# Kernel tuning notes

Hardware: AMD Instinct MI355X
Metric: run time of the kernel (lower is better)

The kernel has to match this reference:

```python
import jax, jax.numpy as jnp
import numpy as np

B, T, D, HEADS = 4, 2048, 2048, 16  # math requires T == D


def setup_inputs() -> dict:
    key = jax.random.key(0)
    k1, k2, k3 = jax.random.split(key, 3)
    scale = 1.0 / np.sqrt(D)
    x = jax.random.normal(k1, (B, T, D), dtype=jnp.float32)
    w_qk = jax.random.normal(k2, (2 * D, D), dtype=jnp.float32) * scale
    w_dense = jax.random.normal(k3, (D, D), dtype=jnp.float32) * scale
    b_dense = jnp.zeros((D,), dtype=jnp.float32)
    return {"x": x, "w_qk": w_qk, "w_dense": w_dense, "b_dense": b_dense}


def reference(x, w_qk, w_dense, b_dense):
    b, t, d = x.shape
    h = HEADS
    vh = d // h
    # to_q_k: Linear(d, 2d, bias=False); chunk into k0, v
    kv = jnp.einsum('btd,ed->bte', x, w_qk)          # [b,t,2d]
    k0, v = kv[..., :d], kv[..., d:]                 # each [b,t,d]
    scale_factor = 1.0 / jnp.sqrt(jnp.asarray(d * (d - 1) / 2, dtype=x.dtype))
    # k = k0.transpose(1,2) -> [b,d,t]; scores = k @ v^T -> [b,d,t] (t==d)
    s = jnp.einsum('bmi,bjm->bij', k0, v) * scale_factor   # [b,d,t]
    a = jax.nn.softmax(s, axis=-1)
    q = jnp.einsum('bit,btd->bid', a, v)             # [b,d,d]
    # q.transpose(0,1).chunk(h, dim=0) -> stack(dim=1) -> transpose(1,2) -> reshape
    qt = jnp.swapaxes(q, 0, 1)                       # [d, b, d]
    stk = qt.reshape(h, vh, b, d)                    # h chunks of [vh,b,d]
    stk = jnp.transpose(stk, (1, 0, 2, 3))           # stack(dim=1): [vh,h,b,d]
    stk = jnp.transpose(stk, (0, 2, 1, 3))           # transpose(1,2): [vh,b,h,d]
    out = stk.reshape(b, t, d)
    # dropout in eval mode == identity; to_dense Linear
    return jnp.einsum('btd,ed->bte', out, w_dense) + b_dense
```

## Files before the change

### kernel.cpp

```cpp
#include <hip/hip_runtime.h>
#include <stdint.h>
#include <math.h>


typedef __bf16 bf16x8 __attribute__((ext_vector_type(8)));
typedef float  f32x4  __attribute__((ext_vector_type(4)));

typedef __attribute__((address_space(3))) uint32_t lds_u32_t;
typedef __attribute__((address_space(1))) const uint32_t glb_u32_t;

__device__ __forceinline__ float bf2f(uint16_t u) {
  union { uint32_t i; float f; } c; c.i = ((uint32_t)u) << 16; return c.f;
}
__device__ __forceinline__ uint16_t f2bf(float f) {
  union { float f; uint32_t i; } c; c.f = f;
  uint32_t i = c.i;
  return (uint16_t)((i + 0x7fffu + ((i >> 16) & 1u)) >> 16);
}

__device__ __forceinline__ void glds16(const uint16_t* g, const char* l) {
  __builtin_amdgcn_global_load_lds((glb_u32_t*)g, (lds_u32_t*)l, 16, 0, 0);
}

#define SCHED0() __builtin_amdgcn_sched_barrier(0)
#define BARRIER() do { SCHED0(); __builtin_amdgcn_s_barrier(); SCHED0(); } while (0)
#define VMCNT(n_) asm volatile("s_waitcnt vmcnt(" #n_ ")")

#define NX4 4194304u
#define NW4 2097152u
#define ND4 1048576u
__global__ __launch_bounds__(256) void k_cast_all(
    const float* __restrict__ x, const float* __restrict__ wqk,
    const float* __restrict__ wd, uint16_t* __restrict__ dst) {
  uint32_t i = blockIdx.x * 256 + threadIdx.x;
  float4 v;
  if (i < NX4)            v = reinterpret_cast<const float4*>(x)[i];
  else if (i < NX4 + NW4) v = reinterpret_cast<const float4*>(wqk)[i - NX4];
  else                    v = reinterpret_cast<const float4*>(wd)[i - NX4 - NW4];
  ushort4 o;
  o.x = f2bf(v.x); o.y = f2bf(v.y); o.z = f2bf(v.z); o.w = f2bf(v.w);
  reinterpret_cast<ushort4*>(dst)[i] = o;
}

__device__ __forceinline__ void gemm256_core(
    const uint16_t* aR0, const uint16_t* aR1,
    const uint16_t* bR0, const uint16_t* bR1,
    int K, f32x4 acc[8][4])
{
  extern __shared__ uint4 smem_u4[];
  char* smem = (char*)smem_u4;
  const int tid = threadIdx.x;
  const int w = tid >> 6, l = tid & 63;
  const int wm = (w >> 2) * 128, wn = (w & 3) * 64;
  const int frow = l & 15, fkc = l >> 4;
  const uint32_t chunk = (uint32_t)((fkc ^ ((frow >> 1) & 3)) * 16);
  const uint32_t aBase = (uint32_t)(wm + frow) * 64 + chunk;
  const uint32_t bBase = 65536u + (uint32_t)(wn + frow) * 64 + chunk;
  char* lW = smem + (uint32_t)w * 1024u;
  const int NIT = K >> 7;

#define LDSA(kh_, buf_, half_) (lW + ((buf_) * 32768u + (kh_) * 16384u + (half_) * 8192u))
#define LDSB(kh_, buf_, half_) (lW + (65536u + (buf_) * 32768u + (kh_) * 16384u + (half_) * 8192u))
#define STG_A(off_, kh_, buf_) do { \
    glds16(aR0 + (off_), LDSA(kh_, buf_, 0)); \
    glds16(aR1 + (off_), LDSA(kh_, buf_, 1)); } while (0)
#define STG_B(off_, kh_, buf_) do { \
    glds16(bR0 + (off_), LDSB(kh_, buf_, 0)); \
    glds16(bR1 + (off_), LDSB(kh_, buf_, 1)); } while (0)
#define RD_A(mi_, kh_, buf_) \
    (*reinterpret_cast<const bf16x8*>(smem + (aBase + (mi_) * 1024u + (kh_) * 16384u + (buf_) * 32768u)))
#define RD_B(ni_, kh_, buf_) \
    (*reinterpret_cast<const bf16x8*>(smem + (bBase + (ni_) * 1024u + (kh_) * 16384u + (buf_) * 32768u)))
#define PH_RD12(kh_, buf_) do { \
    a0 = RD_A(0, kh_, buf_); a1 = RD_A(1, kh_, buf_); \
    a2 = RD_A(2, kh_, buf_); a3 = RD_A(3, kh_, buf_); \
    a4 = RD_A(4, kh_, buf_); a5 = RD_A(5, kh_, buf_); \
    a6 = RD_A(6, kh_, buf_); a7 = RD_A(7, kh_, buf_); \
    b0 = RD_B(0, kh_, buf_); b1 = RD_B(1, kh_, buf_); \
    b2 = RD_B(2, kh_, buf_); b3 = RD_B(3, kh_, buf_); } while (0)
#define MFMA8(ai_, mi_) do { \
    acc[mi_][0] = __builtin_amdgcn_mfma_f32_16x16x32_bf16(ai_, b0, acc[mi_][0], 0, 0, 0); \
    acc[mi_][1] = __builtin_amdgcn_mfma_f32_16x16x32_bf16(ai_, b1, acc[mi_][1], 0, 0, 0); \
    acc[mi_][2] = __builtin_amdgcn_mfma_f32_16x16x32_bf16(ai_, b2, acc[mi_][2], 0, 0, 0); \
    acc[mi_][3] = __builtin_amdgcn_mfma_f32_16x16x32_bf16(ai_, b3, acc[mi_][3], 0, 0, 0); \
  } while (0)
#define MFMA_PH() do { \
    BARRIER(); \
    __builtin_amdgcn_s_setprio(1); \
    MFMA8(a0, 0); MFMA8(a1, 1); MFMA8(a2, 2); MFMA8(a3, 3); \
    MFMA8(a4, 4); MFMA8(a5, 5); MFMA8(a6, 6); MFMA8(a7, 7); \
    __builtin_amdgcn_s_setprio(0); } while (0)

  STG_A(0, 0, 0); STG_B(0, 0, 0); STG_A(32, 1, 0); STG_B(32, 1, 0);
  STG_A(64, 0, 1); STG_B(64, 0, 1);
  VMCNT(8);

  bf16x8 a0, a1, a2, a3, a4, a5, a6, a7, b0, b1, b2, b3;
  BARRIER();

  for (int it = 0; it < NIT - 1; ++it) {
    PH_RD12(0, 0); STG_A(96, 1, 1);  STG_B(96, 1, 1);  VMCNT(8); MFMA_PH();
    PH_RD12(1, 0); STG_A(128, 0, 0); STG_B(128, 0, 0); VMCNT(8); MFMA_PH();
    PH_RD12(0, 1); STG_A(160, 1, 0); STG_B(160, 1, 0); VMCNT(8); MFMA_PH();
    PH_RD12(1, 1); STG_A(192, 0, 1); STG_B(192, 0, 1); VMCNT(8); MFMA_PH();
    aR0 += 128; aR1 += 128; bR0 += 128; bR1 += 128;
  }

  PH_RD12(0, 0); STG_A(96, 1, 1); STG_B(96, 1, 1); VMCNT(8); MFMA_PH();
  PH_RD12(1, 0); VMCNT(4); MFMA_PH();
  PH_RD12(0, 1); VMCNT(4); MFMA_PH();
  PH_RD12(1, 1); VMCNT(0); MFMA_PH();
#undef LDSA
#undef LDSB
#undef STG_A
#undef STG_B
#undef RD_A
#undef RD_B
#undef PH_RD12
#undef MFMA8
#undef MFMA_PH
}

__device__ __forceinline__ int stage_co() {
  const int tid = threadIdx.x;
  return (((tid & 3) ^ ((tid >> 3) & 3)) * 8);
}

__global__ __launch_bounds__(512, 2) void k_gemm_kv(
    const uint16_t* __restrict__ W,
    const uint16_t* __restrict__ X,
    uint16_t* __restrict__ k0T,
    uint16_t* __restrict__ vT)
{
  const int tid = threadIdx.x;
  const int bm = blockIdx.y, bn = blockIdx.x;
  const int r0 = tid >> 2, co = stage_co();
  const uint16_t* aR0 = W + (size_t)(bm * 256 + r0) * 2048 + co;
  const uint16_t* aR1 = W + (size_t)(bm * 256 + 128 + r0) * 2048 + co;
  const uint16_t* bR0 = X + (size_t)(bn * 256 + r0) * 2048 + co;
  const uint16_t* bR1 = X + (size_t)(bn * 256 + 128 + r0) * 2048 + co;
  f32x4 acc[8][4];
#pragma unroll
  for (int i = 0; i < 8; ++i)
#pragma unroll
    for (int j = 0; j < 4; ++j) acc[i][j] = (f32x4){0.f, 0.f, 0.f, 0.f};
  gemm256_core(aR0, aR1, bR0, bR1, 2048, acc);
  const int w = tid >> 6, l = tid & 63;
  const int wm = (w >> 2) * 128, wn = (w & 3) * 64;
  const int cr = (l >> 4) * 4, cc = l & 15;
  uint16_t* Cb = (bm < 8) ? k0T : vT;
  const int rb = (bm & 7) * 256;
#pragma unroll
  for (int mi = 0; mi < 8; ++mi)
#pragma unroll
    for (int ni = 0; ni < 4; ++ni)
#pragma unroll
      for (int g = 0; g < 4; ++g) {
        int lr = rb + wm + mi * 16 + cr + g;
        int bt = bn * 256 + wn + ni * 16 + cc;
        Cb[(size_t)lr * 8192 + bt] = f2bf(acc[mi][ni][g]);
      }
}

__global__ __launch_bounds__(512, 2) void k_gemm_bt(
    const uint16_t* __restrict__ A, int lda, long sA,
    const uint16_t* __restrict__ B, int ldb, long sB,
    uint16_t* __restrict__ C, int ldc, long sC,
    int K, float scale)
{
  const int z = blockIdx.z;
  A += (size_t)z * sA; B += (size_t)z * sB; C += (size_t)z * sC;
  const int tid = threadIdx.x;
  const int bm = blockIdx.y, bn = blockIdx.x;
  const int r0 = tid >> 2, co = stage_co();
  const uint16_t* aR0 = A + (size_t)(bm * 256 + r0) * lda + co;
  const uint16_t* aR1 = A + (size_t)(bm * 256 + 128 + r0) * lda + co;
  const uint16_t* bR0 = B + (size_t)(bn * 256 + r0) * ldb + co;
  const uint16_t* bR1 = B + (size_t)(bn * 256 + 128 + r0) * ldb + co;
  f32x4 acc[8][4];
#pragma unroll
  for (int i = 0; i < 8; ++i)
#pragma unroll
    for (int j = 0; j < 4; ++j) acc[i][j] = (f32x4){0.f, 0.f, 0.f, 0.f};
  gemm256_core(aR0, aR1, bR0, bR1, K, acc);
  const int w = tid >> 6, l = tid & 63;
  const int wm = (w >> 2) * 128, wn = (w & 3) * 64;
  const int cr = (l >> 4) * 4, cc = l & 15;
#pragma unroll
  for (int mi = 0; mi < 8; ++mi)
#pragma unroll
    for (int ni = 0; ni < 4; ++ni)
#pragma unroll
      for (int g = 0; g < 4; ++g) {
        int grow = bm * 256 + wm + mi * 16 + cr + g;
        int gcol = bn * 256 + wn + ni * 16 + cc;
        C[(size_t)grow * ldc + gcol] = f2bf(acc[mi][ni][g] * scale);
      }
}

__device__ __forceinline__ size_t qrow_off(int rr) {
  int bp = rr >> 11, tp = rr & 2047;
  int bi = (tp >> 4) & 3;
  int i  = (tp & 15) * 128 + bp * 32 + (tp >> 6);
  return ((size_t)bi * 2048 + (size_t)i) * 2048;
}

__global__ __launch_bounds__(512, 2) void k_gemm_out(
    const uint16_t* __restrict__ Q,
    const uint16_t* __restrict__ W,
    const float*    __restrict__ bias,
    float*          __restrict__ Out)
{
  const int tid = threadIdx.x;
  const int bm = blockIdx.y, bn = blockIdx.x;
  const int r0 = tid >> 2, co = stage_co();
  const uint16_t* aR0 = Q + qrow_off(bm * 256 + r0) + co;
  const uint16_t* aR1 = Q + qrow_off(bm * 256 + 128 + r0) + co;
  const uint16_t* bR0 = W + (size_t)(bn * 256 + r0) * 2048 + co;
  const uint16_t* bR1 = W + (size_t)(bn * 256 + 128 + r0) * 2048 + co;
  f32x4 acc[8][4];
#pragma unroll
  for (int i = 0; i < 8; ++i)
#pragma unroll
    for (int j = 0; j < 4; ++j) acc[i][j] = (f32x4){0.f, 0.f, 0.f, 0.f};
  gemm256_core(aR0, aR1, bR0, bR1, 2048, acc);
  const int w = tid >> 6, l = tid & 63;
  const int wm = (w >> 2) * 128, wn = (w & 3) * 64;
  const int cr = (l >> 4) * 4, cc = l & 15;
#pragma unroll
  for (int mi = 0; mi < 8; ++mi)
#pragma unroll
    for (int ni = 0; ni < 4; ++ni)
#pragma unroll
      for (int g = 0; g < 4; ++g) {
        int grow = bm * 256 + wm + mi * 16 + cr + g;
        int gcol = bn * 256 + wn + ni * 16 + cc;
        Out[(size_t)grow * 2048 + gcol] = acc[mi][ni][g] + bias[gcol];
      }
}

__global__ __launch_bounds__(256) void k_transpose(
    const uint16_t* __restrict__ src, uint16_t* __restrict__ dst)
{
  __shared__ uint16_t tile[64][65];
  const int tid = threadIdx.x;
  const int bx = blockIdx.x;
  const int by = blockIdx.y;
  const int cu = tid & 31, r0 = tid >> 5;
#pragma unroll
  for (int p = 0; p < 8; ++p) {
    int r = p * 8 + r0;
    uint32_t v = *reinterpret_cast<const uint32_t*>(
        &src[(size_t)(by * 64 + r) * 8192 + bx * 64 + cu * 2]);
    tile[r][cu * 2]     = (uint16_t)(v & 0xffffu);
    tile[r][cu * 2 + 1] = (uint16_t)(v >> 16);
  }
  __syncthreads();
#pragma unroll
  for (int p = 0; p < 8; ++p) {
    int r = p * 8 + r0;
    uint32_t lo = tile[cu * 2][r], hi = tile[cu * 2 + 1][r];
    *reinterpret_cast<uint32_t*>(
        &dst[(size_t)(bx * 64 + r) * 2048 + by * 64 + cu * 2]) = lo | (hi << 16);
  }
}

__global__ __launch_bounds__(256) void k_softmax(uint16_t* __restrict__ s)
{
  uint16_t* p = s + (size_t)blockIdx.x * 2048;
  const int tid = threadIdx.x;
  uint4 raw = reinterpret_cast<const uint4*>(p)[tid];
  uint32_t u[4] = {raw.x, raw.y, raw.z, raw.w};
  float x[8];
#pragma unroll
  for (int i = 0; i < 4; ++i) {
    x[2 * i]     = bf2f((uint16_t)(u[i] & 0xffffu));
    x[2 * i + 1] = bf2f((uint16_t)(u[i] >> 16));
  }
  float m = x[0];
#pragma unroll
  for (int i = 1; i < 8; ++i) m = fmaxf(m, x[i]);
#pragma unroll
  for (int o = 32; o; o >>= 1) m = fmaxf(m, __shfl_xor(m, o, 64));
  __shared__ float redm[4], reds[4];
  if ((tid & 63) == 0) redm[tid >> 6] = m;
  __syncthreads();
  m = fmaxf(fmaxf(redm[0], redm[1]), fmaxf(redm[2], redm[3]));
  float sum = 0.f;
#pragma unroll
  for (int i = 0; i < 8; ++i) { x[i] = __expf(x[i] - m); sum += x[i]; }
#pragma unroll
  for (int o = 32; o; o >>= 1) sum += __shfl_xor(sum, o, 64);
  if ((tid & 63) == 0) reds[tid >> 6] = sum;
  __syncthreads();
  sum = reds[0] + reds[1] + reds[2] + reds[3];
  float inv = 1.0f / sum;
  uint32_t ou[4];
#pragma unroll
  for (int i = 0; i < 4; ++i) {
    uint32_t lo = f2bf(x[2 * i] * inv);
    uint32_t hi = f2bf(x[2 * i + 1] * inv);
    ou[i] = lo | (hi << 16);
  }
  reinterpret_cast<uint4*>(p)[tid] = make_uint4(ou[0], ou[1], ou[2], ou[3]);
}

extern "C" void kernel_launch(void* const* d_in, const int* in_sizes, int n_in,
                              void* d_out, int out_size, void* d_ws, size_t ws_size,
                              hipStream_t stream) {
  const float* x       = (const float*)d_in[0];
  const float* w_qk    = (const float*)d_in[1];
  const float* w_dense = (const float*)d_in[2];
  const float* b_dense = (const float*)d_in[3];
  float* out = (float*)d_out;

  static int attr_done = 0;
  if (!attr_done) {
    (void)hipFuncSetAttribute(reinterpret_cast<const void*>(k_gemm_kv),
                              hipFuncAttributeMaxDynamicSharedMemorySize, 131072);
    (void)hipFuncSetAttribute(reinterpret_cast<const void*>(k_gemm_bt),
                              hipFuncAttributeMaxDynamicSharedMemorySize, 131072);
    (void)hipFuncSetAttribute(reinterpret_cast<const void*>(k_gemm_out),
                              hipFuncAttributeMaxDynamicSharedMemorySize, 131072);
    attr_done = 1;
  }

  const size_t NX = 4ull * 2048 * 2048;
  const size_t NW = 4096ull * 2048;
  const size_t ND = 2048ull * 2048;

  uint16_t* xb   = (uint16_t*)d_ws;
  uint16_t* wqkb = xb + NX;
  uint16_t* wdb  = wqkb + NW;
  uint16_t* k0T  = wdb + ND;
  uint16_t* vT   = k0T + NX;
  uint16_t* qb   = xb;
  uint16_t* Vn   = (uint16_t*)d_out;
  uint16_t* sb   = Vn + NX;

  const float scale = (float)(1.0 / sqrt(0.5 * 2048.0 * 2047.0));

  k_cast_all<<<dim3((NX4 + NW4 + ND4) / 256), 256, 0, stream>>>(x, w_qk, w_dense, xb);

  k_gemm_kv<<<dim3(32, 16), 512, 131072, stream>>>(wqkb, xb, k0T, vT);
  k_transpose<<<dim3(128, 32), 256, 0, stream>>>(vT, Vn);
  k_gemm_bt<<<dim3(8, 8, 4), 512, 131072, stream>>>(
      k0T, 8192, 2048L, Vn, 2048, 2048L * 2048L, sb, 2048, 2048L * 2048L, 2048, scale);
  k_softmax<<<dim3(8192), 256, 0, stream>>>(sb);
  k_gemm_bt<<<dim3(8, 8, 4), 512, 131072, stream>>>(
      sb, 2048, 2048L * 2048L, vT, 8192, 2048L, qb, 2048, 2048L * 2048L, 2048, 1.0f);
  k_gemm_out<<<dim3(8, 32), 512, 131072, stream>>>(qb, wdb, b_dense, out);
}
```

Baseline: 473.1 us.

## Software-pipeline LDS fragment reads with MFMAs across quarter-K stages in GEMM core

Restructures the 256x256 GEMM main loop so that LDS reads for the next K-slice are interleaved with the MFMAs of the current slice. B fragments are double-buffered in registers and each A fragment is reloaded right after its MFMA group. The staging pattern moves from two buffers of two halves to four quarter buffers, with one barrier per segment. The aim is to hide LDS read latency behind matrix math, at the cost of more live registers, which could pressure occupancy at 2 blocks per CU.

```diff
diff --git a/kernel.cpp b/kernel.cpp
--- a/kernel.cpp
+++ b/kernel.cpp
@@ -57,68 +57,83 @@
   const uint32_t aBase = (uint32_t)(wm + frow) * 64 + chunk;
   const uint32_t bBase = 65536u + (uint32_t)(wn + frow) * 64 + chunk;
   char* lW = smem + (uint32_t)w * 1024u;
-  const int NIT = K >> 7;
-
-#define LDSA(kh_, buf_, half_) (lW + ((buf_) * 32768u + (kh_) * 16384u + (half_) * 8192u))
-#define LDSB(kh_, buf_, half_) (lW + (65536u + (buf_) * 32768u + (kh_) * 16384u + (half_) * 8192u))
-#define STG_A(off_, kh_, buf_) do { \
-    glds16(aR0 + (off_), LDSA(kh_, buf_, 0)); \
-    glds16(aR1 + (off_), LDSA(kh_, buf_, 1)); } while (0)
-#define STG_B(off_, kh_, buf_) do { \
-    glds16(bR0 + (off_), LDSB(kh_, buf_, 0)); \
-    glds16(bR1 + (off_), LDSB(kh_, buf_, 1)); } while (0)
-#define RD_A(mi_, kh_, buf_) \
-    (*reinterpret_cast<const bf16x8*>(smem + (aBase + (mi_) * 1024u + (kh_) * 16384u + (buf_) * 32768u)))
-#define RD_B(ni_, kh_, buf_) \
-    (*reinterpret_cast<const bf16x8*>(smem + (bBase + (ni_) * 1024u + (kh_) * 16384u + (buf_) * 32768u)))
-#define PH_RD12(kh_, buf_) do { \
-    a0 = RD_A(0, kh_, buf_); a1 = RD_A(1, kh_, buf_); \
-    a2 = RD_A(2, kh_, buf_); a3 = RD_A(3, kh_, buf_); \
-    a4 = RD_A(4, kh_, buf_); a5 = RD_A(5, kh_, buf_); \
-    a6 = RD_A(6, kh_, buf_); a7 = RD_A(7, kh_, buf_); \
-    b0 = RD_B(0, kh_, buf_); b1 = RD_B(1, kh_, buf_); \
-    b2 = RD_B(2, kh_, buf_); b3 = RD_B(3, kh_, buf_); } while (0)
-#define MFMA8(ai_, mi_) do { \
-    acc[mi_][0] = __builtin_amdgcn_mfma_f32_16x16x32_bf16(ai_, b0, acc[mi_][0], 0, 0, 0); \
-    acc[mi_][1] = __builtin_amdgcn_mfma_f32_16x16x32_bf16(ai_, b1, acc[mi_][1], 0, 0, 0); \
-    acc[mi_][2] = __builtin_amdgcn_mfma_f32_16x16x32_bf16(ai_, b2, acc[mi_][2], 0, 0, 0); \
-    acc[mi_][3] = __builtin_amdgcn_mfma_f32_16x16x32_bf16(ai_, b3, acc[mi_][3], 0, 0, 0); \
+  const int NIT = (K >> 7) - 1;
+
+#define ROFF(q_) ((uint32_t)((q_) & 1) * 16384u + (uint32_t)((q_) >> 1) * 32768u)
+#define RDA(mi_, q_) \
+    (*reinterpret_cast<const bf16x8*>(smem + (aBase + (mi_) * 1024u + ROFF(q_))))
+#define RDB(ni_, q_) \
+    (*reinterpret_cast<const bf16x8*>(smem + (bBase + (ni_) * 1024u + ROFF(q_))))
+#define RDB4(D0_, D1_, D2_, D3_, q_) do { \
+    D0_ = RDB(0, q_); D1_ = RDB(1, q_); D2_ = RDB(2, q_); D3_ = RDB(3, q_); } while (0)
+#define STG4(off_, q_) do { \
+    glds16(aR0 + (off_), lW + ROFF(q_)); \
+    glds16(aR1 + (off_), lW + (ROFF(q_) + 8192u)); \
+    glds16(bR0 + (off_), lW + (65536u + ROFF(q_))); \
+    glds16(bR1 + (off_), lW + (65536u + ROFF(q_) + 8192u)); } while (0)
+#define MFMA4(ai_, mi_, B0_, B1_, B2_, B3_) do { \
+    acc[mi_][0] = __builtin_amdgcn_mfma_f32_16x16x32_bf16(ai_, B0_, acc[mi_][0], 0, 0, 0); \
+    acc[mi_][1] = __builtin_amdgcn_mfma_f32_16x16x32_bf16(ai_, B1_, acc[mi_][1], 0, 0, 0); \
+    acc[mi_][2] = __builtin_amdgcn_mfma_f32_16x16x32_bf16(ai_, B2_, acc[mi_][2], 0, 0, 0); \
+    acc[mi_][3] = __builtin_amdgcn_mfma_f32_16x16x32_bf16(ai_, B3_, acc[mi_][3], 0, 0, 0); \
   } while (0)
-#define MFMA_PH() do { \
-    BARRIER(); \
+#define CLUST_RD(qn_, B0_, B1_, B2_, B3_) do { \
     __builtin_amdgcn_s_setprio(1); \
-    MFMA8(a0, 0); MFMA8(a1, 1); MFMA8(a2, 2); MFMA8(a3, 3); \
-    MFMA8(a4, 4); MFMA8(a5, 5); MFMA8(a6, 6); MFMA8(a7, 7); \
+    MFMA4(a0, 0, B0_, B1_, B2_, B3_); a0 = RDA(0, qn_); \
+    MFMA4(a1, 1, B0_, B1_, B2_, B3_); a1 = RDA(1, qn_); \
+    MFMA4(a2, 2, B0_, B1_, B2_, B3_); a2 = RDA(2, qn_); \
+    MFMA4(a3, 3, B0_, B1_, B2_, B3_); a3 = RDA(3, qn_); \
+    MFMA4(a4, 4, B0_, B1_, B2_, B3_); a4 = RDA(4, qn_); \
+    MFMA4(a5, 5, B0_, B1_, B2_, B3_); a5 = RDA(5, qn_); \
+    MFMA4(a6, 6, B0_, B1_, B2_, B3_); a6 = RDA(6, qn_); \
+    MFMA4(a7, 7, B0_, B1_, B2_, B3_); a7 = RDA(7, qn_); \
     __builtin_amdgcn_s_setprio(0); } while (0)
-
-  STG_A(0, 0, 0); STG_B(0, 0, 0); STG_A(32, 1, 0); STG_B(32, 1, 0);
-  STG_A(64, 0, 1); STG_B(64, 0, 1);
+#define CLUST_END(B0_, B1_, B2_, B3_) do { \
+    __builtin_amdgcn_s_setprio(1); \
+    MFMA4(a0, 0, B0_, B1_, B2_, B3_); MFMA4(a1, 1, B0_, B1_, B2_, B3_); \
+    MFMA4(a2, 2, B0_, B1_, B2_, B3_); MFMA4(a3, 3, B0_, B1_, B2_, B3_); \
+    MFMA4(a4, 4, B0_, B1_, B2_, B3_); MFMA4(a5, 5, B0_, B1_, B2_, B3_); \
+    MFMA4(a6, 6, B0_, B1_, B2_, B3_); MFMA4(a7, 7, B0_, B1_, B2_, B3_); \
+    __builtin_amdgcn_s_setprio(0); } while (0)
+#define SEG_STD(off_, q_, qn_, BC0, BC1, BC2, BC3, BA0, BA1, BA2, BA3) do { \
+    STG4(off_, q_); \
+    RDB4(BA0, BA1, BA2, BA3, qn_); \
+    CLUST_RD(qn_, BC0, BC1, BC2, BC3); \
+    VMCNT(8); \
+    BARRIER(); } while (0)
+
+  STG4(0, 0); STG4(32, 1); STG4(64, 2); STG4(96, 3);
   VMCNT(8);
-
-  bf16x8 a0, a1, a2, a3, a4, a5, a6, a7, b0, b1, b2, b3;
   BARRIER();
 
-  for (int it = 0; it < NIT - 1; ++it) {
-    PH_RD12(0, 0); STG_A(96, 1, 1);  STG_B(96, 1, 1);  VMCNT(8); MFMA_PH();
-    PH_RD12(1, 0); STG_A(128, 0, 0); STG_B(128, 0, 0); VMCNT(8); MFMA_PH();
-    PH_RD12(0, 1); STG_A(160, 1, 0); STG_B(160, 1, 0); VMCNT(8); MFMA_PH();
-    PH_RD12(1, 1); STG_A(192, 0, 1); STG_B(192, 0, 1); VMCNT(8); MFMA_PH();
+  bf16x8 a0, a1, a2, a3, a4, a5, a6, a7;
+  bf16x8 bx0, bx1, bx2, bx3, by0, by1, by2, by3;
+  RDB4(bx0, bx1, bx2, bx3, 0);
+  a0 = RDA(0, 0); a1 = RDA(1, 0); a2 = RDA(2, 0); a3 = RDA(3, 0);
+  a4 = RDA(4, 0); a5 = RDA(5, 0); a6 = RDA(6, 0); a7 = RDA(7, 0);
+  BARRIER();
+
+  for (int it = 0; it < NIT; ++it) {
+    SEG_STD(128, 0, 1, bx0, bx1, bx2, bx3, by0, by1, by2, by3);
+    SEG_STD(160, 1, 2, by0, by1, by2, by3, bx0, bx1, bx2, bx3);
+    SEG_STD(192, 2, 3, bx0, bx1, bx2, bx3, by0, by1, by2, by3);
+    SEG_STD(224, 3, 0, by0, by1, by2, by3, bx0, bx1, bx2, bx3);
     aR0 += 128; aR1 += 128; bR0 += 128; bR1 += 128;
   }
 
-  PH_RD12(0, 0); STG_A(96, 1, 1); STG_B(96, 1, 1); VMCNT(8); MFMA_PH();
-  PH_RD12(1, 0); VMCNT(4); MFMA_PH();
-  PH_RD12(0, 1); VMCNT(4); MFMA_PH();
-  PH_RD12(1, 1); VMCNT(0); MFMA_PH();
-#undef LDSA
-#undef LDSB
-#undef STG_A
-#undef STG_B
-#undef RD_A
-#undef RD_B
-#undef PH_RD12
-#undef MFMA8
-#undef MFMA_PH
+  RDB4(by0, by1, by2, by3, 1); CLUST_RD(1, bx0, bx1, bx2, bx3); VMCNT(4); BARRIER();
+  RDB4(bx0, bx1, bx2, bx3, 2); CLUST_RD(2, by0, by1, by2, by3); VMCNT(0); BARRIER();
+  RDB4(by0, by1, by2, by3, 3); CLUST_RD(3, bx0, bx1, bx2, bx3);
+  CLUST_END(by0, by1, by2, by3);
+#undef ROFF
+#undef RDA
+#undef RDB
+#undef RDB4
+#undef STG4
+#undef MFMA4
+#undef CLUST_RD
+#undef CLUST_END
+#undef SEG_STD
 }
 
 __device__ __forceinline__ int stage_co() {
```

Result: slower. 589.2 us (+24.5%).
